# Performance work log

Measured on AMD Instinct MI355X. Metric: run time of the kernel, lower is better.

The kernel has to match this reference:

```python
import jax, jax.numpy as jnp
import numpy as np

NUM_HEADS = 12


def setup_inputs() -> dict:
    key = jax.random.key(0)
    k1, k2, k3, k4 = jax.random.split(key, 4)
    B, N, C = 8, 1024, 768
    x = jax.random.normal(k1, (B, N, C), dtype=jnp.float32)
    w_qkv = jax.random.normal(k2, (3 * C, C), dtype=jnp.float32) * 0.02
    w_proj = jax.random.normal(k3, (C, C), dtype=jnp.float32) * 0.02
    b_proj = jax.random.normal(k4, (C,), dtype=jnp.float32) * 0.02
    return {"x": x, "w_qkv": w_qkv, "w_proj": w_proj, "b_proj": b_proj}


def reference(x, w_qkv, w_proj, b_proj):
    B, N, C = x.shape
    H = NUM_HEADS
    D = C // H
    scale = D ** -0.5
    # qkv projection (HMQLinear with quant=False is a plain linear, bias=False)
    qkv = jnp.einsum('bnc,oc->bno', x, w_qkv)          # [B,N,3C]
    qkv = qkv.reshape(B, N, 3, H, D).transpose(2, 0, 3, 1, 4)  # [3,B,H,N,D]
    q, k, v = qkv[0], qkv[1], qkv[2]
    # HMQMulQK (passthrough matmul), scale applied after QK^T as in source
    attn = jnp.einsum('bhqd,bhkd->bhqk', q, k) * scale  # [B,H,N,N]
    attn = jax.nn.softmax(attn, axis=-1)                # HMQSoftmax
    out = jnp.einsum('bhqk,bhkd->bhqd', attn, v)        # HMQMulSV
    out = out.transpose(0, 2, 1, 3).reshape(B, N, C)
    # output projection (HMQLinear, default bias=True)
    return jnp.einsum('bnc,oc->bno', out, w_proj) + b_proj
```

## Files before the change

### kernel.cpp

```cpp
#include <hip/hip_runtime.h>
#include <hip/hip_bf16.h>
#include <stdint.h>

typedef __attribute__((ext_vector_type(8))) short short8;
typedef __attribute__((ext_vector_type(4))) float f32x4;
typedef __attribute__((ext_vector_type(16))) float f32x16;
typedef __attribute__((ext_vector_type(4))) unsigned short us4;

#define AS1 __attribute__((address_space(1)))
#define AS3 __attribute__((address_space(3)))

__device__ inline unsigned short f2bf(float f) {
    unsigned int u = __float_as_uint(f);
    u += 0x7FFFu + ((u >> 16) & 1u);
    return (unsigned short)(u >> 16);
}

__device__ inline unsigned int cvtpk(float lo, float hi) {
    unsigned int r;
    asm("v_cvt_pk_bf16_f32 %0, %1, %2" : "=v"(r) : "v"(lo), "v"(hi));
    return r;
}

__device__ inline void pl32swap(unsigned int& a, unsigned int& b) {
    asm volatile("v_permlane32_swap_b32 %0, %1" : "+v"(a), "+v"(b));
}

__device__ inline float fexp2(float x) {
#if __has_builtin(__builtin_amdgcn_exp2f)
    return __builtin_amdgcn_exp2f(x);
#else
    return exp2f(x);
#endif
}

#define VMW(N) asm volatile("s_waitcnt vmcnt(" #N ")" ::: "memory")
#define BARR() __builtin_amdgcn_s_barrier()

__global__ void cvt_all(const float* __restrict__ x, const float* __restrict__ wq,
                        const float* __restrict__ wp,
                        unsigned short* __restrict__ xb,
                        unsigned short* __restrict__ wqb,
                        unsigned short* __restrict__ wpb) {
    const int X4 = 1572864, Q4 = 442368;
    int i = blockIdx.x * blockDim.x + threadIdx.x;
    const float* src; unsigned short* dst; int j;
    if (i < X4) { src = x; dst = xb; j = i; }
    else if (i < X4 + Q4) { src = wq; dst = wqb; j = i - X4; }
    else { src = wp; dst = wpb; j = i - X4 - Q4; }
    float4 v = ((const float4*)src)[j];
    us4 o;
    o.x = f2bf(v.x); o.y = f2bf(v.y); o.z = f2bf(v.z); o.w = f2bf(v.w);
    ((us4*)dst)[j] = o;
}

#define BM 128
#define BN 128

template<int MODE>
__global__ __launch_bounds__(256)
void gemm_bt(const unsigned short* __restrict__ A,
             const unsigned short* __restrict__ Bm,
             unsigned short* __restrict__ Qo, unsigned short* __restrict__ Ko,
             unsigned short* __restrict__ Vto,
             float* __restrict__ Co, const float* __restrict__ bias,
             int M, int N, int K)
{
    __shared__ __align__(16) unsigned short As[2][BM * 64];
    __shared__ __align__(16) unsigned short Bs[2][BM * 64];
    const int tid = threadIdx.x;
    const int wave = tid >> 6, lane = tid & 63;
    const int tr = blockIdx.x * BM;
    const int tc = blockIdx.y * BN;
    const int wm = wave >> 1, wn = wave & 1;

    f32x4 acc[4][4] = {};

    auto stage = [&](int it, int buf) {
#pragma unroll
        for (int i = 0; i < 4; ++i) {
            int cid = i * 256 + tid;
            int r = cid >> 3, cd = cid & 7;
            int sc = cd ^ (r & 7);
            __builtin_amdgcn_global_load_lds(
                (const AS1 void*)(A + (size_t)(tr + r) * K + it * 64 + sc * 8),
                (AS3 void*)(&As[buf][(i * 256 + wave * 64) * 8]), 16, 0, 0);
            __builtin_amdgcn_global_load_lds(
                (const AS1 void*)(Bm + (size_t)(tc + r) * K + it * 64 + sc * 8),
                (AS3 void*)(&Bs[buf][(i * 256 + wave * 64) * 8]), 16, 0, 0);
        }
    };

    const int nIt = K / 64;
    stage(0, 0);

    for (int it = 0; it < nIt; ++it) {
        const int cur = it & 1;
        if (it + 1 < nIt) { stage(it + 1, cur ^ 1); VMW(8); }
        else              { VMW(0); }
        BARR();

#pragma unroll
        for (int kh = 0; kh < 2; ++kh) {
            short8 af[4], bfr[4];
#pragma unroll
            for (int mt = 0; mt < 4; ++mt) {
                int rr = wm * 64 + mt * 16 + (lane & 15);
                int c = kh * 4 + (lane >> 4);
                af[mt] = *(const short8*)&As[cur][rr * 64 + ((c ^ (rr & 7)) * 8)];
            }
#pragma unroll
            for (int nt = 0; nt < 4; ++nt) {
                int rr = wn * 64 + nt * 16 + (lane & 15);
                int c = kh * 4 + (lane >> 4);
                bfr[nt] = *(const short8*)&Bs[cur][rr * 64 + ((c ^ (rr & 7)) * 8)];
            }
#pragma unroll
            for (int mt = 0; mt < 4; ++mt)
#pragma unroll
                for (int nt = 0; nt < 4; ++nt)
                    acc[mt][nt] = __builtin_amdgcn_mfma_f32_16x16x32_bf16(af[mt], bfr[nt], acc[mt][nt], 0, 0, 0);
        }

        BARR();
    }

    const float QSCALE = 0.18033688011112042f;
#pragma unroll
    for (int mt = 0; mt < 4; ++mt) {
#pragma unroll
        for (int nt = 0; nt < 4; ++nt) {
            int col = tc + wn * 64 + nt * 16 + (lane & 15);
            int row0 = tr + wm * 64 + mt * 16 + (lane >> 4) * 4;
            if constexpr (MODE == 0) {
                int s = (col >= 1536) ? 2 : (col >= 768 ? 1 : 0);
                int rem = col - s * 768;
                int h = rem >> 6, d = rem & 63;
                int b = row0 >> 10, n0 = row0 & 1023;
                int bh = b * 12 + h;
                if (s == 2) {
                    us4 pv;
#pragma unroll
                    for (int r = 0; r < 4; ++r) pv[r] = f2bf(acc[mt][nt][r]);
                    int qd = (n0 >> 2) & 3;
                    int nst = n0 + ((qd == 1) ? 4 : (qd == 2) ? -4 : 0);
                    *(us4*)&Vto[((size_t)bh * 64 + d) * 1024 + nst] = pv;
                } else {
                    unsigned short* dst = (s == 0) ? Qo : Ko;
                    float sc = (s == 0) ? QSCALE : 1.0f;
#pragma unroll
                    for (int r = 0; r < 4; ++r)
                        dst[((size_t)bh * 1024 + n0 + r) * 64 + d] = f2bf(acc[mt][nt][r] * sc);
                }
            } else {
#pragma unroll
                for (int r = 0; r < 4; ++r)
                    Co[(size_t)(row0 + r) * N + col] = acc[mt][nt][r] + bias[col];
            }
        }
    }
}

__global__ __launch_bounds__(256, 3)
void attn_kernel(const unsigned short* __restrict__ Q,
                 const unsigned short* __restrict__ Kg,
                 const unsigned short* __restrict__ Vt,
                 unsigned short* __restrict__ Og)
{
    __shared__ __align__(16) unsigned short KV[3][2][64 * 64];

    const int tid = threadIdx.x;
    const int wave = tid >> 6, lane = tid & 63;
    const int l31 = lane & 31, hi = lane >> 5;

    const int id = blockIdx.x;
    const int swz = (id & 7) * 96 + (id >> 3);
    const int bh = swz >> 3, qb = swz & 7;

    const int b = bh / 12, h = bh % 12;
    const size_t baseK = (size_t)bh * 1024 * 64;
    const size_t baseV = (size_t)bh * 64 * 1024;
    const int q0 = qb * 128 + wave * 32;

    short8 qf[4];
#pragma unroll
    for (int ds = 0; ds < 4; ++ds)
        qf[ds] = *(const short8*)&Q[baseK + (size_t)(q0 + l31) * 64 + ds * 16 + hi * 8];

    f32x16 ot0 = {}, ot1 = {};
    float l = 0.f;

    auto stage = [&](int kt, int buf) {
        const unsigned short* gK = Kg + baseK + (size_t)kt * 64 * 64;
        const unsigned short* gV = Vt + baseV + kt * 64;
#pragma unroll
        for (int i = 0; i < 2; ++i) {
            int c = wave * 128 + i * 64 + lane;
            int r = c >> 3, cc = c & 7;
            int sw = (cc ^ (r & 7)) * 8;
            __builtin_amdgcn_global_load_lds(
                (const AS1 void*)(gK + r * 64 + sw),
                (AS3 void*)(&KV[buf][0][(wave * 128 + i * 64) * 8]), 16, 0, 0);
            __builtin_amdgcn_global_load_lds(
                (const AS1 void*)(gV + (size_t)r * 1024 + sw),
                (AS3 void*)(&KV[buf][1][(wave * 128 + i * 64) * 8]), 16, 0, 0);
        }
    };

    auto rfrag = [&](const unsigned short* s, int row, int cc) -> short8 {
        return *(const short8*)&s[(row * 8 + (cc ^ (row & 7))) * 8];
    };

    auto pack8 = [&](const f32x16& S, int r0) -> short8 {
        union { unsigned int u[4]; short8 s; } fr;
#pragma unroll
        for (int w = 0; w < 4; ++w)
            fr.u[w] = cvtpk(S[r0 + 2 * w], S[r0 + 2 * w + 1]);
        return fr.s;
    };

    stage(0, 0);
    stage(1, 1);
    int cb = 0, sb = 2;

    for (int kt = 0; kt < 16; ++kt) {
        if (kt < 15) { VMW(4); }
        else         { VMW(0); }
        BARR();
        if (kt < 14) stage(kt + 2, sb);

        f32x16 st0 = {}, st1 = {};
        __builtin_amdgcn_s_setprio(1);
#pragma unroll
        for (int ds = 0; ds < 4; ++ds) {
            short8 k0 = rfrag(KV[cb][0], l31, ds * 2 + hi);
            short8 k1 = rfrag(KV[cb][0], 32 + l31, ds * 2 + hi);
            st0 = __builtin_amdgcn_mfma_f32_32x32x16_bf16(k0, qf[ds], st0, 0, 0, 0);
            st1 = __builtin_amdgcn_mfma_f32_32x32x16_bf16(k1, qf[ds], st1, 0, 0, 0);
        }
        __builtin_amdgcn_s_setprio(0);

        short8 v00 = rfrag(KV[cb][1], l31, 0 + hi);
        short8 v10 = rfrag(KV[cb][1], 32 + l31, 0 + hi);
        short8 v01 = rfrag(KV[cb][1], l31, 2 + hi);
        short8 v11 = rfrag(KV[cb][1], 32 + l31, 2 + hi);

#pragma unroll
        for (int i = 0; i < 16; ++i) st0[i] = fexp2(st0[i]);
        short8 paf0 = pack8(st0, 0);
        short8 paf1 = pack8(st0, 8);

        __builtin_amdgcn_s_setprio(1);
        ot0 = __builtin_amdgcn_mfma_f32_32x32x16_bf16(v00, paf0, ot0, 0, 0, 0);
        ot1 = __builtin_amdgcn_mfma_f32_32x32x16_bf16(v10, paf0, ot1, 0, 0, 0);
        ot0 = __builtin_amdgcn_mfma_f32_32x32x16_bf16(v01, paf1, ot0, 0, 0, 0);
        ot1 = __builtin_amdgcn_mfma_f32_32x32x16_bf16(v11, paf1, ot1, 0, 0, 0);
        __builtin_amdgcn_s_setprio(0);

        short8 v02 = rfrag(KV[cb][1], l31, 4 + hi);
        short8 v12 = rfrag(KV[cb][1], 32 + l31, 4 + hi);
        short8 v03 = rfrag(KV[cb][1], l31, 6 + hi);
        short8 v13 = rfrag(KV[cb][1], 32 + l31, 6 + hi);
#pragma unroll
        for (int i = 0; i < 16; ++i) st1[i] = fexp2(st1[i]);
        short8 paf2 = pack8(st1, 0);
        short8 paf3 = pack8(st1, 8);

        __builtin_amdgcn_s_setprio(1);
        ot0 = __builtin_amdgcn_mfma_f32_32x32x16_bf16(v02, paf2, ot0, 0, 0, 0);
        ot1 = __builtin_amdgcn_mfma_f32_32x32x16_bf16(v12, paf2, ot1, 0, 0, 0);
        ot0 = __builtin_amdgcn_mfma_f32_32x32x16_bf16(v03, paf3, ot0, 0, 0, 0);
        ot1 = __builtin_amdgcn_mfma_f32_32x32x16_bf16(v13, paf3, ot1, 0, 0, 0);
        __builtin_amdgcn_s_setprio(0);

        float su[8];
#pragma unroll
        for (int i = 0; i < 8; ++i)
            su[i] = (st0[2 * i] + st0[2 * i + 1]) + (st1[2 * i] + st1[2 * i + 1]);
#pragma unroll
        for (int s = 4; s > 0; s >>= 1)
#pragma unroll
            for (int i = 0; i < 4; ++i)
                if (i < s) su[i] += su[i + s];
        l += su[0];

        cb = (cb == 2) ? 0 : cb + 1;
        sb = (sb == 2) ? 0 : sb + 1;
    }

    {
        unsigned int pu = __float_as_uint(l), pv = pu;
        pl32swap(pu, pv);
        l += __uint_as_float(hi ? pv : pu);
    }

    float inv = 1.f / l;
#pragma unroll
    for (int i = 0; i < 16; ++i) { ot0[i] *= inv; ot1[i] *= inv; }

    BARR();

    unsigned int* ow = (unsigned int*)(&KV[0][0][0]) + wave * 1152;
#pragma unroll
    for (int dt = 0; dt < 2; ++dt)
#pragma unroll
        for (int rp = 0; rp < 8; ++rp) {
            unsigned int w = (dt == 0) ? cvtpk(ot0[2 * rp], ot0[2 * rp + 1])
                                       : cvtpk(ot1[2 * rp], ot1[2 * rp + 1]);
            int wd = dt * 16 + 4 * (rp >> 1) + 2 * hi + (rp & 1);
            ow[l31 * 36 + wd] = w;
        }
#pragma unroll
    for (int i = 0; i < 4; ++i) {
        int c = i * 64 + lane;
        int qr = c >> 3, ch = c & 7;
        short8 vv = *(const short8*)((const unsigned short*)&ow[qr * 36 + ch * 4]);
        *(short8*)&Og[(size_t)(b * 1024 + q0 + qr) * 768 + h * 64 + ch * 8] = vv;
    }
}

extern "C" void kernel_launch(void* const* d_in, const int* in_sizes, int n_in,
                              void* d_out, int out_size, void* d_ws, size_t ws_size,
                              hipStream_t stream) {
    const float* x      = (const float*)d_in[0];
    const float* w_qkv  = (const float*)d_in[1];
    const float* w_proj = (const float*)d_in[2];
    const float* b_proj = (const float*)d_in[3];
    float* out = (float*)d_out;

    const int Bb = 8, Nn = 1024, C = 768;
    const int M = Bb * Nn;
    const size_t XB = (size_t)M * C;
    const size_t WQ = (size_t)3 * C * C;
    const size_t WP = (size_t)C * C;
    const size_t QE = (size_t)96 * 1024 * 64;

    unsigned short* xb  = (unsigned short*)d_ws;
    unsigned short* wqb = xb + XB;
    unsigned short* wpb = wqb + WQ;
    unsigned short* Qb  = wpb + WP;
    unsigned short* Kb  = Qb + QE;
    unsigned short* Vtb = Kb + QE;
    unsigned short* AO  = Vtb + QE;

    cvt_all<<<8448, 256, 0, stream>>>(x, w_qkv, w_proj, xb, wqb, wpb);

    gemm_bt<0><<<dim3(M / BM, (3 * C) / BN), 256, 0, stream>>>(
        xb, wqb, Qb, Kb, Vtb, nullptr, nullptr, M, 3 * C, C);

    attn_kernel<<<768, 256, 0, stream>>>(Qb, Kb, Vtb, AO);

    gemm_bt<1><<<dim3(M / BM, C / BN), 256, 0, stream>>>(
        AO, wpb, nullptr, nullptr, nullptr, out, b_proj, M, C, C);
}
```

Baseline: 109.5 us.

## Use a 256x256 tile, 8-wave QKV GEMM with quadrant-phased pipelined loads

Replaces the QKV projection's 128x128 tile kernel with a dedicated 512-thread kernel computing 256x256 output tiles. Each tile is split into four 128x128 quadrant phases, and each phase issues the next k-step's global-to-LDS load for one A or B half. The MFMA bursts run at raised wave priority. The aim is to raise operand reuse per byte loaded and hide load latency behind compute, at the cost of more LDS (128 KB) and registers per block and fewer blocks in the grid (288).

Result: slower. 129.0 us (+17.8%).

```diff
diff --git a/kernel.cpp b/kernel.cpp
--- a/kernel.cpp
+++ b/kernel.cpp
@@ -35,6 +35,8 @@
 }
 
 #define VMW(N) asm volatile("s_waitcnt vmcnt(" #N ")" ::: "memory")
+#define LGK0() do { asm volatile("s_waitcnt lgkmcnt(0)" ::: "memory"); \
+                    __builtin_amdgcn_sched_barrier(0); } while (0)
 #define BARR() __builtin_amdgcn_s_barrier()
 
 __global__ void cvt_all(const float* __restrict__ x, const float* __restrict__ wq,
@@ -54,17 +56,138 @@
     ((us4*)dst)[j] = o;
 }
 
+__global__ __launch_bounds__(512, 2)
+void qkv_gemm(const unsigned short* __restrict__ Ag,
+              const unsigned short* __restrict__ Bg,
+              unsigned short* __restrict__ Qo, unsigned short* __restrict__ Ko,
+              unsigned short* __restrict__ Vto)
+{
+    __shared__ __align__(16) unsigned short ldsA[2][2][128 * 64];
+    __shared__ __align__(16) unsigned short ldsB[2][2][128 * 64];
+    const int tid = threadIdx.x;
+    const int wave = tid >> 6, lane = tid & 63;
+    const int wm = wave >> 2, wn = wave & 3;
+    const int tr = blockIdx.x * 256, tc = blockIdx.y * 256;
+    const int K = 768;
+
+    f32x4 acc[2][2][4][2] = {};
+
+    auto stgA = [&](int t, int bf, int mh) {
+#pragma unroll
+        for (int i = 0; i < 2; ++i) {
+            int cid = i * 512 + tid;
+            int r = cid >> 3, cd = cid & 7;
+            int sc = cd ^ (r & 7);
+            __builtin_amdgcn_global_load_lds(
+                (const AS1 void*)(Ag + (size_t)(tr + mh * 128 + r) * K + t * 64 + sc * 8),
+                (AS3 void*)(&ldsA[bf][mh][(i * 512 + wave * 64) * 8]), 16, 0, 0);
+        }
+    };
+    auto stgB = [&](int t, int bf, int nh) {
+#pragma unroll
+        for (int i = 0; i < 2; ++i) {
+            int cid = i * 512 + tid;
+            int r = cid >> 3, cd = cid & 7;
+            int sc = cd ^ (r & 7);
+            __builtin_amdgcn_global_load_lds(
+                (const AS1 void*)(Bg + (size_t)(tc + nh * 128 + r) * K + t * 64 + sc * 8),
+                (AS3 void*)(&ldsB[bf][nh][(i * 512 + wave * 64) * 8]), 16, 0, 0);
+        }
+    };
+
+#define QPHASE(B_, MH, NH, STG)                                               \
+    {                                                                         \
+        short8 af[4][2], bfr[2][2];                                           \
+        _Pragma("unroll") for (int mt = 0; mt < 4; ++mt)                      \
+            _Pragma("unroll") for (int kk = 0; kk < 2; ++kk) {                \
+                int lr = wm * 64 + mt * 16 + (lane & 15);                     \
+                int pc = (kk * 4 + (lane >> 4)) ^ (lr & 7);                   \
+                af[mt][kk] = *(const short8*)&ldsA[B_][MH][lr * 64 + pc * 8]; \
+            }                                                                 \
+        _Pragma("unroll") for (int nt = 0; nt < 2; ++nt)                      \
+            _Pragma("unroll") for (int kk = 0; kk < 2; ++kk) {                \
+                int lr = wn * 32 + nt * 16 + (lane & 15);                     \
+                int pc = (kk * 4 + (lane >> 4)) ^ (lr & 7);                   \
+                bfr[nt][kk] = *(const short8*)&ldsB[B_][NH][lr * 64 + pc * 8];\
+            }                                                                 \
+        STG;                                                                  \
+        LGK0();                                                               \
+        __builtin_amdgcn_s_setprio(1);                                        \
+        _Pragma("unroll") for (int mt = 0; mt < 4; ++mt)                      \
+            _Pragma("unroll") for (int nt = 0; nt < 2; ++nt) {                \
+                acc[MH][NH][mt][nt] = __builtin_amdgcn_mfma_f32_16x16x32_bf16(\
+                    af[mt][0], bfr[nt][0], acc[MH][NH][mt][nt], 0, 0, 0);     \
+                acc[MH][NH][mt][nt] = __builtin_amdgcn_mfma_f32_16x16x32_bf16(\
+                    af[mt][1], bfr[nt][1], acc[MH][NH][mt][nt], 0, 0, 0);     \
+            }                                                                 \
+        __builtin_amdgcn_s_setprio(0);                                        \
+    }
+
+    stgA(0, 0, 0); stgB(0, 0, 0); stgB(0, 0, 1); stgA(0, 0, 1);
+
+    for (int t = 0; t < 11; ++t) {
+        const int b = t & 1, nb = b ^ 1;
+        VMW(4); BARR();
+        QPHASE(b, 0, 0, stgA(t + 1, nb, 0));
+        VMW(4); BARR();
+        QPHASE(b, 0, 1, stgB(t + 1, nb, 0));
+        VMW(4); BARR();
+        QPHASE(b, 1, 0, stgB(t + 1, nb, 1));
+        BARR();
+        QPHASE(b, 1, 1, stgA(t + 1, nb, 1));
+    }
+    VMW(4); BARR();
+    QPHASE(1, 0, 0, (void)0);
+    VMW(2); BARR();
+    QPHASE(1, 0, 1, (void)0);
+    VMW(0); BARR();
+    QPHASE(1, 1, 0, (void)0);
+    BARR();
+    QPHASE(1, 1, 1, (void)0);
+#undef QPHASE
+
+    const float QSCALE = 0.18033688011112042f;
+    const int s = blockIdx.y / 3;
+#pragma unroll
+    for (int mh = 0; mh < 2; ++mh)
+#pragma unroll
+    for (int nh = 0; nh < 2; ++nh)
+#pragma unroll
+    for (int mt = 0; mt < 4; ++mt)
+#pragma unroll
+    for (int nt = 0; nt < 2; ++nt) {
+        int col = tc + wn * 32 + nh * 128 + nt * 16 + (lane & 15);
+        int row0 = tr + wm * 64 + mh * 128 + mt * 16 + (lane >> 4) * 4;
+        int rem = col - s * 768;
+        int h = rem >> 6, d = rem & 63;
+        int bb = row0 >> 10, n0 = row0 & 1023;
+        int bh = bb * 12 + h;
+        f32x4 v = acc[mh][nh][mt][nt];
+        if (s == 2) {
+            us4 pv;
+#pragma unroll
+            for (int r = 0; r < 4; ++r) pv[r] = f2bf(v[r]);
+            int qd = (n0 >> 2) & 3;
+            int nst = n0 + ((qd == 1) ? 4 : (qd == 2) ? -4 : 0);
+            *(us4*)&Vto[((size_t)bh * 64 + d) * 1024 + nst] = pv;
+        } else {
+            unsigned short* dst = s ? Ko : Qo;
+            float sc2 = s ? 1.0f : QSCALE;
+#pragma unroll
+            for (int r = 0; r < 4; ++r)
+                dst[((size_t)bh * 1024 + n0 + r) * 64 + d] = f2bf(v[r] * sc2);
+        }
+    }
+}
+
 #define BM 128
 #define BN 128
 
-template<int MODE>
 __global__ __launch_bounds__(256)
-void gemm_bt(const unsigned short* __restrict__ A,
-             const unsigned short* __restrict__ Bm,
-             unsigned short* __restrict__ Qo, unsigned short* __restrict__ Ko,
-             unsigned short* __restrict__ Vto,
-             float* __restrict__ Co, const float* __restrict__ bias,
-             int M, int N, int K)
+void proj_gemm(const unsigned short* __restrict__ A,
+               const unsigned short* __restrict__ Bm,
+               float* __restrict__ Co, const float* __restrict__ bias,
+               int M, int N, int K)
 {
     __shared__ __align__(16) unsigned short As[2][BM * 64];
     __shared__ __align__(16) unsigned short Bs[2][BM * 64];
@@ -125,40 +248,16 @@
         BARR();
     }
 
-    const float QSCALE = 0.18033688011112042f;
-#pragma unroll
-    for (int mt = 0; mt < 4; ++mt) {
+#pragma unroll
+    for (int mt = 0; mt < 4; ++mt)
 #pragma unroll
         for (int nt = 0; nt < 4; ++nt) {
             int col = tc + wn * 64 + nt * 16 + (lane & 15);
             int row0 = tr + wm * 64 + mt * 16 + (lane >> 4) * 4;
-            if constexpr (MODE == 0) {
-                int s = (col >= 1536) ? 2 : (col >= 768 ? 1 : 0);
-                int rem = col - s * 768;
-                int h = rem >> 6, d = rem & 63;
-                int b = row0 >> 10, n0 = row0 & 1023;
-                int bh = b * 12 + h;
-                if (s == 2) {
-                    us4 pv;
-#pragma unroll
-                    for (int r = 0; r < 4; ++r) pv[r] = f2bf(acc[mt][nt][r]);
-                    int qd = (n0 >> 2) & 3;
-                    int nst = n0 + ((qd == 1) ? 4 : (qd == 2) ? -4 : 0);
-                    *(us4*)&Vto[((size_t)bh * 64 + d) * 1024 + nst] = pv;
-                } else {
-                    unsigned short* dst = (s == 0) ? Qo : Ko;
-                    float sc = (s == 0) ? QSCALE : 1.0f;
-#pragma unroll
-                    for (int r = 0; r < 4; ++r)
-                        dst[((size_t)bh * 1024 + n0 + r) * 64 + d] = f2bf(acc[mt][nt][r] * sc);
-                }
-            } else {
-#pragma unroll
-                for (int r = 0; r < 4; ++r)
-                    Co[(size_t)(row0 + r) * N + col] = acc[mt][nt][r] + bias[col];
-            }
-        }
-    }
+#pragma unroll
+            for (int r = 0; r < 4; ++r)
+                Co[(size_t)(row0 + r) * N + col] = acc[mt][nt][r] + bias[col];
+        }
 }
 
 __global__ __launch_bounds__(256, 3)
@@ -345,11 +444,11 @@
 
     cvt_all<<<8448, 256, 0, stream>>>(x, w_qkv, w_proj, xb, wqb, wpb);
 
-    gemm_bt<0><<<dim3(M / BM, (3 * C) / BN), 256, 0, stream>>>(
-        xb, wqb, Qb, Kb, Vtb, nullptr, nullptr, M, 3 * C, C);
+    qkv_gemm<<<dim3(M / 256, (3 * C) / 256), 512, 0, stream>>>(
+        xb, wqb, Qb, Kb, Vtb);
 
     attn_kernel<<<768, 256, 0, stream>>>(Qb, Kb, Vtb, AO);
 
-    gemm_bt<1><<<dim3(M / BM, C / BN), 256, 0, stream>>>(
-        AO, wpb, nullptr, nullptr, nullptr, out, b_proj, M, C, C);
-}
+    proj_gemm<<<dim3(M / BM, C / BN), 256, 0, stream>>>(
+        AO, wpb, out, b_proj, M, C, C);
+}
```

## Fuse fp32-to-bf16 conversion of x into the QKV GEMM A-tile load

Applied to the files above, without the earlier changes.

Removes the separate conversion pass over x. The QKV GEMM now loads fp32 x rows into registers, packs them to bf16 and writes them into swizzled shared memory, software-pipelined two iterations ahead. The weight matrices are still converted by a smaller kernel. This saves a full write and read of bf16 x, but each column block re-reads fp32 x, which doubles A-operand global traffic and adds register pressure. The main loop also now uses wait-count pipelining and MFMA priority hints.

Result: slower. 174.0 us (+58.9%).

```diff
diff --git a/kernel.cpp b/kernel.cpp
--- a/kernel.cpp
+++ b/kernel.cpp
@@ -6,6 +6,7 @@
 typedef __attribute__((ext_vector_type(4))) float f32x4;
 typedef __attribute__((ext_vector_type(16))) float f32x16;
 typedef __attribute__((ext_vector_type(4))) unsigned short us4;
+typedef __attribute__((ext_vector_type(4))) unsigned int u32x4;
 
 #define AS1 __attribute__((address_space(1)))
 #define AS3 __attribute__((address_space(3)))
@@ -14,6 +15,13 @@
     unsigned int u = __float_as_uint(f);
     u += 0x7FFFu + ((u >> 16) & 1u);
     return (unsigned short)(u >> 16);
+}
+
+__device__ inline unsigned int pk_rne(float a, float b) {
+    unsigned int ua = __float_as_uint(a), ub = __float_as_uint(b);
+    ua += 0x7FFFu + ((ua >> 16) & 1u);
+    ub += 0x7FFFu + ((ub >> 16) & 1u);
+    return (ua >> 16) | (ub & 0xFFFF0000u);
 }
 
 __device__ inline unsigned int cvtpk(float lo, float hi) {
@@ -35,19 +43,17 @@
 }
 
 #define VMW(N) asm volatile("s_waitcnt vmcnt(" #N ")" ::: "memory")
+#define LGKW0() asm volatile("s_waitcnt lgkmcnt(0)" ::: "memory")
 #define BARR() __builtin_amdgcn_s_barrier()
 
-__global__ void cvt_all(const float* __restrict__ x, const float* __restrict__ wq,
-                        const float* __restrict__ wp,
-                        unsigned short* __restrict__ xb,
-                        unsigned short* __restrict__ wqb,
-                        unsigned short* __restrict__ wpb) {
-    const int X4 = 1572864, Q4 = 442368;
+__global__ void cvt_w(const float* __restrict__ wq, const float* __restrict__ wp,
+                      unsigned short* __restrict__ wqb,
+                      unsigned short* __restrict__ wpb) {
+    const int Q4 = 442368;
     int i = blockIdx.x * blockDim.x + threadIdx.x;
     const float* src; unsigned short* dst; int j;
-    if (i < X4) { src = x; dst = xb; j = i; }
-    else if (i < X4 + Q4) { src = wq; dst = wqb; j = i - X4; }
-    else { src = wp; dst = wpb; j = i - X4 - Q4; }
+    if (i < Q4) { src = wq; dst = wqb; j = i; }
+    else        { src = wp; dst = wpb; j = i - Q4; }
     float4 v = ((const float4*)src)[j];
     us4 o;
     o.x = f2bf(v.x); o.y = f2bf(v.y); o.z = f2bf(v.z); o.w = f2bf(v.w);
@@ -57,14 +63,144 @@
 #define BM 128
 #define BN 128
 
-template<int MODE>
 __global__ __launch_bounds__(256)
-void gemm_bt(const unsigned short* __restrict__ A,
-             const unsigned short* __restrict__ Bm,
-             unsigned short* __restrict__ Qo, unsigned short* __restrict__ Ko,
-             unsigned short* __restrict__ Vto,
-             float* __restrict__ Co, const float* __restrict__ bias,
-             int M, int N, int K)
+void qkv_gemm(const float* __restrict__ X,
+              const unsigned short* __restrict__ Bm,
+              unsigned short* __restrict__ Qo, unsigned short* __restrict__ Ko,
+              unsigned short* __restrict__ Vto)
+{
+    __shared__ __align__(16) unsigned short As[2][BM * 64];
+    __shared__ __align__(16) unsigned short Bs[2][BM * 64];
+    const int tid = threadIdx.x;
+    const int wave = tid >> 6, lane = tid & 63;
+    const int tr = blockIdx.x * BM;
+    const int tc = blockIdx.y * BN;
+    const int wm = wave >> 1, wn = wave & 1;
+    const int K = 768;
+
+    f32x4 acc[4][4] = {};
+
+    const int ar = tid >> 1, ah = tid & 1;
+    const float* xrow = X + (size_t)(tr + ar) * K + ah * 32;
+
+    f32x4 areg[8];
+    auto loadA = [&](int it) {
+#pragma unroll
+        for (int j = 0; j < 8; ++j)
+            areg[j] = *(const f32x4*)(xrow + it * 64 + j * 4);
+    };
+    auto writeA = [&](int buf) {
+#pragma unroll
+        for (int j2 = 0; j2 < 4; ++j2) {
+            u32x4 w;
+            w.x = pk_rne(areg[2 * j2][0], areg[2 * j2][1]);
+            w.y = pk_rne(areg[2 * j2][2], areg[2 * j2][3]);
+            w.z = pk_rne(areg[2 * j2 + 1][0], areg[2 * j2 + 1][1]);
+            w.w = pk_rne(areg[2 * j2 + 1][2], areg[2 * j2 + 1][3]);
+            int cd = ah * 4 + j2;
+            *(u32x4*)&As[buf][ar * 64 + ((cd ^ (ar & 7)) * 8)] = w;
+        }
+    };
+    auto stageB = [&](int it, int buf) {
+#pragma unroll
+        for (int i = 0; i < 4; ++i) {
+            int cid = i * 256 + tid;
+            int r = cid >> 3, cd = cid & 7;
+            int sc = cd ^ (r & 7);
+            __builtin_amdgcn_global_load_lds(
+                (const AS1 void*)(Bm + (size_t)(tc + r) * K + it * 64 + sc * 8),
+                (AS3 void*)(&Bs[buf][(i * 256 + wave * 64) * 8]), 16, 0, 0);
+        }
+    };
+
+    const int nIt = K / 64;
+    loadA(0);
+    stageB(0, 0);
+    VMW(4);
+    writeA(0);
+    loadA(1);
+    LGKW0();
+
+    for (int it = 0; it < nIt; ++it) {
+        const int b = it & 1, nb = b ^ 1;
+        if (it + 1 < nIt) { VMW(8); }
+        else              { VMW(0); }
+        BARR();
+
+        short8 af[4][2], bfr[4][2];
+#pragma unroll
+        for (int mt = 0; mt < 4; ++mt)
+#pragma unroll
+            for (int kh = 0; kh < 2; ++kh) {
+                int rr = wm * 64 + mt * 16 + (lane & 15);
+                int c = kh * 4 + (lane >> 4);
+                af[mt][kh] = *(const short8*)&As[b][rr * 64 + ((c ^ (rr & 7)) * 8)];
+            }
+#pragma unroll
+        for (int nt = 0; nt < 4; ++nt)
+#pragma unroll
+            for (int kh = 0; kh < 2; ++kh) {
+                int rr = wn * 64 + nt * 16 + (lane & 15);
+                int c = kh * 4 + (lane >> 4);
+                bfr[nt][kh] = *(const short8*)&Bs[b][rr * 64 + ((c ^ (rr & 7)) * 8)];
+            }
+
+        if (it + 1 < nIt) {
+            VMW(0);
+            writeA(nb);
+            stageB(it + 1, nb);
+            if (it + 2 < nIt) loadA(it + 2);
+        }
+
+        __builtin_amdgcn_s_setprio(1);
+#pragma unroll
+        for (int kh = 0; kh < 2; ++kh)
+#pragma unroll
+            for (int mt = 0; mt < 4; ++mt)
+#pragma unroll
+                for (int nt = 0; nt < 4; ++nt)
+                    acc[mt][nt] = __builtin_amdgcn_mfma_f32_16x16x32_bf16(af[mt][kh], bfr[nt][kh], acc[mt][nt], 0, 0, 0);
+        __builtin_amdgcn_s_setprio(0);
+
+        LGKW0();
+        BARR();
+    }
+
+    const float QSCALE = 0.18033688011112042f;
+#pragma unroll
+    for (int mt = 0; mt < 4; ++mt) {
+#pragma unroll
+        for (int nt = 0; nt < 4; ++nt) {
+            int col = tc + wn * 64 + nt * 16 + (lane & 15);
+            int row0 = tr + wm * 64 + mt * 16 + (lane >> 4) * 4;
+            int s = (col >= 1536) ? 2 : (col >= 768 ? 1 : 0);
+            int rem = col - s * 768;
+            int h = rem >> 6, d = rem & 63;
+            int b = row0 >> 10, n0 = row0 & 1023;
+            int bh = b * 12 + h;
+            if (s == 2) {
+                us4 pv;
+#pragma unroll
+                for (int r = 0; r < 4; ++r) pv[r] = f2bf(acc[mt][nt][r]);
+                int qd = (n0 >> 2) & 3;
+                int nst = n0 + ((qd == 1) ? 4 : (qd == 2) ? -4 : 0);
+                *(us4*)&Vto[((size_t)bh * 64 + d) * 1024 + nst] = pv;
+            } else {
+                unsigned short* dst = (s == 0) ? Qo : Ko;
+                float sc = (s == 0) ? QSCALE : 1.0f;
+#pragma unroll
+                for (int r = 0; r < 4; ++r)
+                    dst[((size_t)bh * 1024 + n0 + r) * 64 + d] = f2bf(acc[mt][nt][r] * sc);
+            }
+        }
+    }
+}
+
+__global__ __launch_bounds__(256)
+void proj_gemm(const unsigned short* __restrict__ A,
+               const unsigned short* __restrict__ Bm,
+               float* __restrict__ Co, const float* __restrict__ bias,
+               int M, int N, int K)
 {
     __shared__ __align__(16) unsigned short As[2][BM * 64];
     __shared__ __align__(16) unsigned short Bs[2][BM * 64];
@@ -125,40 +261,16 @@
         BARR();
     }
 
-    const float QSCALE = 0.18033688011112042f;
-#pragma unroll
-    for (int mt = 0; mt < 4; ++mt) {
+#pragma unroll
+    for (int mt = 0; mt < 4; ++mt)
 #pragma unroll
         for (int nt = 0; nt < 4; ++nt) {
             int col = tc + wn * 64 + nt * 16 + (lane & 15);
             int row0 = tr + wm * 64 + mt * 16 + (lane >> 4) * 4;
-            if constexpr (MODE == 0) {
-                int s = (col >= 1536) ? 2 : (col >= 768 ? 1 : 0);
-                int rem = col - s * 768;
-                int h = rem >> 6, d = rem & 63;
-                int b = row0 >> 10, n0 = row0 & 1023;
-                int bh = b * 12 + h;
-                if (s == 2) {
-                    us4 pv;
-#pragma unroll
-                    for (int r = 0; r < 4; ++r) pv[r] = f2bf(acc[mt][nt][r]);
-                    int qd = (n0 >> 2) & 3;
-                    int nst = n0 + ((qd == 1) ? 4 : (qd == 2) ? -4 : 0);
-                    *(us4*)&Vto[((size_t)bh * 64 + d) * 1024 + nst] = pv;
-                } else {
-                    unsigned short* dst = (s == 0) ? Qo : Ko;
-                    float sc = (s == 0) ? QSCALE : 1.0f;
-#pragma unroll
-                    for (int r = 0; r < 4; ++r)
-                        dst[((size_t)bh * 1024 + n0 + r) * 64 + d] = f2bf(acc[mt][nt][r] * sc);
-                }
-            } else {
-#pragma unroll
-                for (int r = 0; r < 4; ++r)
-                    Co[(size_t)(row0 + r) * N + col] = acc[mt][nt][r] + bias[col];
-            }
-        }
-    }
+#pragma unroll
+            for (int r = 0; r < 4; ++r)
+                Co[(size_t)(row0 + r) * N + col] = acc[mt][nt][r] + bias[col];
+        }
 }
 
 __global__ __launch_bounds__(256, 3)
@@ -330,26 +442,24 @@
 
     const int Bb = 8, Nn = 1024, C = 768;
     const int M = Bb * Nn;
-    const size_t XB = (size_t)M * C;
     const size_t WQ = (size_t)3 * C * C;
     const size_t WP = (size_t)C * C;
     const size_t QE = (size_t)96 * 1024 * 64;
 
-    unsigned short* xb  = (unsigned short*)d_ws;
-    unsigned short* wqb = xb + XB;
+    unsigned short* wqb = (unsigned short*)d_ws;
     unsigned short* wpb = wqb + WQ;
     unsigned short* Qb  = wpb + WP;
     unsigned short* Kb  = Qb + QE;
     unsigned short* Vtb = Kb + QE;
     unsigned short* AO  = Vtb + QE;
 
-    cvt_all<<<8448, 256, 0, stream>>>(x, w_qkv, w_proj, xb, wqb, wpb);
-
-    gemm_bt<0><<<dim3(M / BM, (3 * C) / BN), 256, 0, stream>>>(
-        xb, wqb, Qb, Kb, Vtb, nullptr, nullptr, M, 3 * C, C);
+    cvt_w<<<2304, 256, 0, stream>>>(w_qkv, w_proj, wqb, wpb);
+
+    qkv_gemm<<<dim3(M / BM, (3 * C) / BN), 256, 0, stream>>>(
+        x, wqb, Qb, Kb, Vtb);
 
     attn_kernel<<<768, 256, 0, stream>>>(Qb, Kb, Vtb, AO);
 
-    gemm_bt<1><<<dim3(M / BM, C / BN), 256, 0, stream>>>(
-        AO, wpb, nullptr, nullptr, nullptr, out, b_proj, M, C, C);
-}
+    proj_gemm<<<dim3(M / BM, C / BN), 256, 0, stream>>>(
+        AO, wpb, out, b_proj, M, C, C);
+}
```

## Load GEMM B operand directly into registers and raise MFMA priority

Applied to the files above, without the earlier changes.

The B tile no longer goes through shared memory. Each wave now reads its B fragments straight from global memory into double-buffered registers. The K loop is unrolled by two to alternate the A LDS buffers and the B register sets. MFMA blocks are wrapped in s_setprio to favour issue. This halves LDS traffic and LDS footprint, at the cost of more VGPRs and duplicate global B reads across waves that share the same columns.

New measurement: 149.6 us. +36.6%, slower.

```diff
diff --git a/kernel.cpp b/kernel.cpp
--- a/kernel.cpp
+++ b/kernel.cpp
@@ -67,7 +67,6 @@
              int M, int N, int K)
 {
     __shared__ __align__(16) unsigned short As[2][BM * 64];
-    __shared__ __align__(16) unsigned short Bs[2][BM * 64];
     const int tid = threadIdx.x;
     const int wave = tid >> 6, lane = tid & 63;
     const int tr = blockIdx.x * BM;
@@ -76,7 +75,9 @@
 
     f32x4 acc[4][4] = {};
 
-    auto stage = [&](int it, int buf) {
+    const unsigned short* Brow = Bm + (size_t)(tc + wn * 64 + (lane & 15)) * K + ((lane >> 4) * 8);
+
+    auto stageA = [&](int it, int buf) {
 #pragma unroll
         for (int i = 0; i < 4; ++i) {
             int cid = i * 256 + tid;
@@ -85,43 +86,52 @@
             __builtin_amdgcn_global_load_lds(
                 (const AS1 void*)(A + (size_t)(tr + r) * K + it * 64 + sc * 8),
                 (AS3 void*)(&As[buf][(i * 256 + wave * 64) * 8]), 16, 0, 0);
-            __builtin_amdgcn_global_load_lds(
-                (const AS1 void*)(Bm + (size_t)(tc + r) * K + it * 64 + sc * 8),
-                (AS3 void*)(&Bs[buf][(i * 256 + wave * 64) * 8]), 16, 0, 0);
-        }
-    };
-
-    const int nIt = K / 64;
-    stage(0, 0);
-
-    for (int it = 0; it < nIt; ++it) {
-        const int cur = it & 1;
-        if (it + 1 < nIt) { stage(it + 1, cur ^ 1); VMW(8); }
-        else              { VMW(0); }
-        BARR();
-
+        }
+    };
+    auto loadB = [&](int it, short8 (&dst)[4][2]) {
+#pragma unroll
+        for (int nt = 0; nt < 4; ++nt)
+#pragma unroll
+            for (int kh = 0; kh < 2; ++kh)
+                dst[nt][kh] = *(const short8*)(Brow + (size_t)(nt * 16) * K + it * 64 + kh * 32);
+    };
+    auto body = [&](int t, int buf, const short8 (&bset)[4][2]) {
 #pragma unroll
         for (int kh = 0; kh < 2; ++kh) {
-            short8 af[4], bfr[4];
+            short8 af[4];
 #pragma unroll
             for (int mt = 0; mt < 4; ++mt) {
                 int rr = wm * 64 + mt * 16 + (lane & 15);
                 int c = kh * 4 + (lane >> 4);
-                af[mt] = *(const short8*)&As[cur][rr * 64 + ((c ^ (rr & 7)) * 8)];
+                af[mt] = *(const short8*)&As[buf][rr * 64 + ((c ^ (rr & 7)) * 8)];
             }
-#pragma unroll
-            for (int nt = 0; nt < 4; ++nt) {
-                int rr = wn * 64 + nt * 16 + (lane & 15);
-                int c = kh * 4 + (lane >> 4);
-                bfr[nt] = *(const short8*)&Bs[cur][rr * 64 + ((c ^ (rr & 7)) * 8)];
-            }
+            __builtin_amdgcn_s_setprio(1);
 #pragma unroll
             for (int mt = 0; mt < 4; ++mt)
 #pragma unroll
                 for (int nt = 0; nt < 4; ++nt)
-                    acc[mt][nt] = __builtin_amdgcn_mfma_f32_16x16x32_bf16(af[mt], bfr[nt], acc[mt][nt], 0, 0, 0);
-        }
-
+                    acc[mt][nt] = __builtin_amdgcn_mfma_f32_16x16x32_bf16(af[mt], bset[nt][kh], acc[mt][nt], 0, 0, 0);
+            __builtin_amdgcn_s_setprio(0);
+        }
+    };
+
+    const int nIt = K / 64;
+    short8 bA[4][2], bB[4][2];
+    stageA(0, 0);
+    loadB(0, bA);
+
+    for (int t = 0; t < nIt; t += 2) {
+        if (t + 1 < nIt) { stageA(t + 1, 1); VMW(4); }
+        else             { VMW(0); }
+        BARR();
+        if (t + 1 < nIt) loadB(t + 1, bB);
+        body(t, 0, bA);
+        BARR();
+        if (t + 2 < nIt) { stageA(t + 2, 0); VMW(4); }
+        else             { VMW(0); }
+        BARR();
+        if (t + 2 < nIt) loadB(t + 2, bA);
+        body(t + 1, 1, bB);
         BARR();
     }
 
```
